# Kernel tuning notes

Measured on AMD Instinct MI355X. Metric: run time of the kernel, lower is better.

## Reference

```python
import jax, jax.numpy as jnp
import numpy as np
import math

MAX_DEGREE = 20
K = (MAX_DEGREE + 1) ** 2  # 441
RANK = 256
N = 262144


def _spharm_all(inc, azim):
    """Real spherical harmonics Y_lm(inc, azim) for all l<=MAX_DEGREE, -l<=m<=l.
    Matches the standard real SH used by get_spherical_harmonics_element:
      Y_l0  = N_l0 * P_l^0(cos inc)
      Y_lm  = sqrt(2) * N_lm * P_l^m(cos inc) * cos(m*azim),  m>0
      Y_l-m = sqrt(2) * N_lm * P_l^m(cos inc) * sin(m*azim),  m>0
    with Condon-Shortley phase folded into the associated Legendre recurrence.
    Output layout: index l*(l+1)+m (the flax index map of the module).
    Returns [..., K]."""
    x = jnp.cos(inc)
    s = jnp.sin(inc)
    # Associated Legendre P_l^m(x) via standard recurrences (trace-time loops,
    # fused by XLA into one elementwise program).
    P = {(0, 0): jnp.ones_like(x)}
    for m in range(1, MAX_DEGREE + 1):
        P[(m, m)] = -(2 * m - 1) * s * P[(m - 1, m - 1)]  # Condon-Shortley
    for m in range(0, MAX_DEGREE):
        P[(m + 1, m)] = (2 * m + 1) * x * P[(m, m)]
    for m in range(0, MAX_DEGREE + 1):
        for l in range(m + 2, MAX_DEGREE + 1):
            P[(l, m)] = ((2 * l - 1) * x * P[(l - 1, m)] - (l + m - 1) * P[(l - 2, m)]) / (l - m)

    cols = [None] * K
    for l in range(MAX_DEGREE + 1):
        for m in range(-l, l + 1):
            am = abs(m)
            norm = math.sqrt((2 * l + 1) / (4.0 * math.pi)
                             * math.factorial(l - am) / math.factorial(l + am))
            if m == 0:
                y = norm * P[(l, 0)]
            elif m > 0:
                y = (math.sqrt(2.0) * norm) * P[(l, am)] * jnp.cos(am * azim)
            else:
                y = (math.sqrt(2.0) * norm) * P[(l, am)] * jnp.sin(am * azim)
            cols[l * (l + 1) + m] = y
    return jnp.stack(cols, axis=-1)


def _cart2sphere(O):
    # returns (azimuth, inclination) of 3-vectors O[..., 3]
    r = jnp.linalg.norm(O, axis=-1)
    azim = jnp.arctan2(O[..., 1], O[..., 0])
    inc = jnp.arccos(jnp.clip(O[..., 2] / r, -1.0, 1.0))
    return azim, inc


def setup_inputs() -> dict:
    key = jax.random.key(0)
    k1, k2, k3 = jax.random.split(key, 3)
    coordinates = jax.random.normal(k1, (N, 6), dtype=jnp.float32)
    rand_i = jax.random.randint(k2, (RANK,), 0, K, dtype=jnp.int32)
    rand_j = jax.random.randint(k3, (RANK,), 0, K, dtype=jnp.int32)
    return {"coordinates": coordinates, "rand_i": rand_i, "rand_j": rand_j}


def reference(coordinates, rand_i, rand_j):
    a1, i1 = _cart2sphere(coordinates[..., :3])
    a2, i2 = _cart2sphere(coordinates[..., 3:])
    Psi_1 = _spharm_all(i1, a1)  # [..., K]
    Psi_2 = _spharm_all(i2, a2)  # [..., K]
    # rank random (i,j) pairs: gathered elementwise product -> [..., RANK]
    return jnp.take(Psi_1, rand_i, axis=-1) * jnp.take(Psi_2, rand_j, axis=-1)
```

## Files before the change

### kernel.cpp

```cpp
#include <hip/hip_runtime.h>
#include <math.h>

#define MAXDEG 20
#define NM 21
#define RANK 256
#define PPB 12
#define NSLOT (2*PPB)
#define S_STRIDE 446
#define HDRS 65


__device__ __forceinline__ int remap_idx(int k) {
  int l = (int)sqrtf((float)k);
  if (l*l > k) --l;
  if ((l+1)*(l+1) <= k) ++l;
  int m = k - l*(l+1);
  int am = m < 0 ? -m : m;
  if (am == 0) return 420 + l;
  return (am-1)*(42-am) + 2*(l-am) + (m < 0 ? 1 : 0);
}

__global__ __launch_bounds__(256, 3)
void sh_fused(const float* __restrict__ coords,
              const int* __restrict__ rand_i,
              const int* __restrict__ rand_j,
              float* __restrict__ out, int N) {
  __shared__ float2 s_ab[231];
  __shared__ float  s_hdr[NSLOT * HDRS];
  __shared__ float  s_tab[NSLOT * S_STRIDE];

  const int t  = threadIdx.x;
  const int n0 = blockIdx.x * PPB;

  const int ri = remap_idx(rand_i[t]);
  const int rj = remap_idx(rand_j[t]);

  if (t < 231) {
    int l = (int)((sqrtf(8.0f*(float)t + 1.0f) - 1.0f) * 0.5f);
    if (l*(l+1)/2 > t) --l;
    if ((l+1)*(l+2)/2 <= t) ++l;
    int m = t - l*(l+1)/2;
    float a = 0.f, b = 0.f;
    if (l >= m + 2) {
      float l2 = (float)(l*l), m2 = (float)(m*m);
      float inv = 1.0f / (l2 - m2);
      a = sqrtf((4.f*l2 - 1.f) * inv);
      b = sqrtf((2.f*(float)l + 1.f) * ((float)((l-1)*(l-1)) - m2)
                / (2.f*(float)l - 3.f) * inv);
    }
    s_ab[t] = make_float2(a, b);
  }

  if (t < NSLOT) {
    int p = t >> 1, d = t & 1;
    int n = n0 + p; if (n >= N) n = N - 1;
    const float* c = coords + (size_t)n * 6 + d * 3;
    float cx = c[0], cy = c[1], cz = c[2];
    float r2 = cx*cx + cy*cy + cz*cz;
    float x = cz * rsqrtf(r2);
    x = fminf(1.f, fmaxf(-1.f, x));
    float s = sqrtf(fmaxf(0.f, 1.f - x*x));
    float rho2 = cx*cx + cy*cy;
    float cphi, sphi;
    if (rho2 > 0.f) { float ir = rsqrtf(rho2); cphi = cx*ir; sphi = cy*ir; }
    else            { cphi = 1.f; sphi = 0.f; }
    float* h = s_hdr + t * HDRS;
    float cm = 1.f, sm = 0.f;
    float pmm = 0.28209479177387814f;
    h[0] = 1.f; h[21] = 0.f; h[42] = pmm; h[63] = x;
    for (int m = 1; m <= MAXDEG; ++m) {
      float cn = cm*cphi - sm*sphi;
      float sn = sm*cphi + cm*sphi;
      cm = cn; sm = sn;
      float df = -sqrtf((2.f*(float)m + 1.f) / (2.f*(float)m));
      if (m == 1) df *= 1.41421356237309515f;
      pmm = df * s * pmm;
      h[m] = cm; h[21+m] = sm; h[42+m] = pmm;
    }
  }
  __syncthreads();

  for (int task = t; task < NM * NSLOT; task += 256) {
    int m  = task / NSLOT;
    int pd = task - m * NSLOT;
    const float* h = s_hdr + pd * HDRS;
    float x  = h[63];
    float cm = h[m], sm = h[21+m], p1 = h[42+m];
    float* slot = s_tab + pd * S_STRIDE;
    if (m == 0) {
      float* col = slot + 420;
      col[0] = p1;
      float p2 = p1;
      float p = 1.7320508075688772f * x * p1;
      col[1] = p;
      int ti = 3;
      for (int l = 2; l <= MAXDEG; ++l) {
        float2 ab = s_ab[ti];
        float pn = ab.x * (x * p) - ab.y * p2;
        p2 = p; p = pn;
        col[l] = pn;
        ti += l + 1;
      }
    } else {
      float2* col = (float2*)(slot + (m-1)*(42-m));
      col[0] = make_float2(p1*cm, p1*sm);
      if (m < MAXDEG) {
        float p2 = p1;
        float p = sqrtf(2.f*(float)m + 3.f) * x * p1;
        col[1] = make_float2(p*cm, p*sm);
        int ti = (m+2)*(m+3)/2 + m;
        for (int l = m+2; l <= MAXDEG; ++l) {
          float2 ab = s_ab[ti];
          float pn = ab.x * (x * p) - ab.y * p2;
          p2 = p; p = pn;
          col[l-m] = make_float2(pn*cm, pn*sm);
          ti += l + 1;
        }
      }
    }
  }
  __syncthreads();

  for (int p = 0; p < PPB; ++p) {
    int n = n0 + p;
    if (n < N) {
      float v = s_tab[(2*p)*S_STRIDE + ri] * s_tab[(2*p+1)*S_STRIDE + rj];
      out[(size_t)n * RANK + t] = v;
    }
  }
}

extern "C" void kernel_launch(void* const* d_in, const int* in_sizes, int n_in,
                              void* d_out, int out_size, void* d_ws, size_t ws_size,
                              hipStream_t stream) {
  const float* coords = (const float*)d_in[0];
  const int*   rand_i = (const int*)d_in[1];
  const int*   rand_j = (const int*)d_in[2];
  float*       out    = (float*)d_out;
  const int N = in_sizes[0] / 6;
  const int grid = (N + PPB - 1) / PPB;
  sh_fused<<<grid, 256, 0, stream>>>(coords, rand_i, rand_j, out, N);
}
```

Before: 394.0 us.

## Parallelize header setup per m, pair Legendre chains, vectorize output stores

Reduces points per block from 12 to 8 and raises the launch-bounds occupancy hint. The serial per-slot header recurrence (cos/sin and P_mm) is replaced by closed forms (atan2 plus sincos of m*phi, and exp2 of m*log2(s)), so all threads compute headers in parallel instead of 16 threads looping over m. Each thread now runs two Legendre chains, one for each direction of a point, and the output is written as float4 using four remapped indices per thread. This cuts the serial prologue and widens the global stores, at the cost of fast-math approximations (__sincosf, exp2/log2) that may lose accuracy at higher m.

After: 437.4 us. +11.0%, slower.

```diff
diff --git a/kernel.cpp b/kernel.cpp
--- a/kernel.cpp
+++ b/kernel.cpp
@@ -4,7 +4,7 @@
 #define MAXDEG 20
 #define NM 21
 #define RANK 256
-#define PPB 12
+#define PPB 8
 #define NSLOT (2*PPB)
 #define S_STRIDE 446
 #define HDRS 65
@@ -20,7 +20,7 @@
   return (am-1)*(42-am) + 2*(l-am) + (m < 0 ? 1 : 0);
 }
 
-__global__ __launch_bounds__(256, 3)
+__global__ __launch_bounds__(256, 4)
 void sh_fused(const float* __restrict__ coords,
               const int* __restrict__ rand_i,
               const int* __restrict__ rand_j,
@@ -32,8 +32,14 @@
   const int t  = threadIdx.x;
   const int n0 = blockIdx.x * PPB;
 
-  const int ri = remap_idx(rand_i[t]);
-  const int rj = remap_idx(rand_j[t]);
+  const int rg = t & 63;
+  int rI[4], rJ[4];
+  {
+    int4 a = ((const int4*)rand_i)[rg];
+    int4 b = ((const int4*)rand_j)[rg];
+    rI[0]=remap_idx(a.x); rI[1]=remap_idx(a.y); rI[2]=remap_idx(a.z); rI[3]=remap_idx(a.w);
+    rJ[0]=remap_idx(b.x); rJ[1]=remap_idx(b.y); rJ[2]=remap_idx(b.z); rJ[3]=remap_idx(b.w);
+  }
 
   if (t < 231) {
     int l = (int)((sqrtf(8.0f*(float)t + 1.0f) - 1.0f) * 0.5f);
@@ -51,82 +57,98 @@
     s_ab[t] = make_float2(a, b);
   }
 
-  if (t < NSLOT) {
-    int p = t >> 1, d = t & 1;
+  {
+    const int slot = t & 15;
+    const int p = slot >> 1, d = slot & 1;
     int n = n0 + p; if (n >= N) n = N - 1;
     const float* c = coords + (size_t)n * 6 + d * 3;
     float cx = c[0], cy = c[1], cz = c[2];
-    float r2 = cx*cx + cy*cy + cz*cz;
-    float x = cz * rsqrtf(r2);
+    float x = cz * rsqrtf(cx*cx + cy*cy + cz*cz);
     x = fminf(1.f, fmaxf(-1.f, x));
     float s = sqrtf(fmaxf(0.f, 1.f - x*x));
-    float rho2 = cx*cx + cy*cy;
-    float cphi, sphi;
-    if (rho2 > 0.f) { float ir = rsqrtf(rho2); cphi = cx*ir; sphi = cy*ir; }
-    else            { cphi = 1.f; sphi = 0.f; }
-    float* h = s_hdr + t * HDRS;
-    float cm = 1.f, sm = 0.f;
-    float pmm = 0.28209479177387814f;
-    h[0] = 1.f; h[21] = 0.f; h[42] = pmm; h[63] = x;
-    for (int m = 1; m <= MAXDEG; ++m) {
-      float cn = cm*cphi - sm*sphi;
-      float sn = sm*cphi + cm*sphi;
-      cm = cn; sm = sn;
-      float df = -sqrtf((2.f*(float)m + 1.f) / (2.f*(float)m));
-      if (m == 1) df *= 1.41421356237309515f;
-      pmm = df * s * pmm;
-      h[m] = cm; h[21+m] = sm; h[42+m] = pmm;
+    s = fmaxf(s, 1e-30f);
+    float phi = atan2f(cy, cx);
+    float l2s = log2f(s);
+    float* h = s_hdr + slot * HDRS;
+    if ((t >> 4) == 0) h[63] = x;
+    for (int m = (t >> 4); m < NM; m += 16) {
+      float sv, cv;
+      __sincosf((float)m * phi, &sv, &cv);
+      float prod = 1.f;
+      for (int k = 1; k <= m; ++k) prod *= (2.f*(float)k + 1.f) / (2.f*(float)k);
+      float Km = 0.28209479177387814f * sqrtf(prod);
+      if (m > 0) { Km *= 1.41421356237309515f; if (m & 1) Km = -Km; }
+      float pmm = Km * exp2f((float)m * l2s);
+      h[m] = cv; h[21 + m] = sv; h[42 + m] = pmm;
     }
   }
   __syncthreads();
 
-  for (int task = t; task < NM * NSLOT; task += 256) {
-    int m  = task / NSLOT;
-    int pd = task - m * NSLOT;
-    const float* h = s_hdr + pd * HDRS;
-    float x  = h[63];
-    float cm = h[m], sm = h[21+m], p1 = h[42+m];
-    float* slot = s_tab + pd * S_STRIDE;
+  if (t < NM * PPB) {
+    const int m = t >> 3, p = t & 7;
+    const float* h0 = s_hdr + (2*p) * HDRS;
+    const float* h1 = h0 + HDRS;
+    float x0 = h0[63],   x1 = h1[63];
+    float cm0 = h0[m],   sm0 = h0[21+m], pm0 = h0[42+m];
+    float cm1 = h1[m],   sm1 = h1[21+m], pm1 = h1[42+m];
+    float* slot0 = s_tab + (2*p) * S_STRIDE;
+    float* slot1 = slot0 + S_STRIDE;
     if (m == 0) {
-      float* col = slot + 420;
-      col[0] = p1;
-      float p2 = p1;
-      float p = 1.7320508075688772f * x * p1;
-      col[1] = p;
+      float* c0 = slot0 + 420; float* c1 = slot1 + 420;
+      float q0 = pm0, q1 = pm1;
+      c0[0] = q0; c1[0] = q1;
+      float p0 = 1.7320508075688772f * x0 * q0;
+      float p1 = 1.7320508075688772f * x1 * q1;
+      c0[1] = p0; c1[1] = p1;
       int ti = 3;
       for (int l = 2; l <= MAXDEG; ++l) {
         float2 ab = s_ab[ti];
-        float pn = ab.x * (x * p) - ab.y * p2;
-        p2 = p; p = pn;
-        col[l] = pn;
+        float v0 = ab.x * (x0 * p0) - ab.y * q0;
+        float v1 = ab.x * (x1 * p1) - ab.y * q1;
+        q0 = p0; p0 = v0; q1 = p1; p1 = v1;
+        c0[l] = v0; c1[l] = v1;
         ti += l + 1;
       }
     } else {
-      float2* col = (float2*)(slot + (m-1)*(42-m));
-      col[0] = make_float2(p1*cm, p1*sm);
+      const int cb = (m-1)*(42-m);
+      float2* c0 = (float2*)(slot0 + cb);
+      float2* c1 = (float2*)(slot1 + cb);
+      c0[0] = make_float2(pm0*cm0, pm0*sm0);
+      c1[0] = make_float2(pm1*cm1, pm1*sm1);
       if (m < MAXDEG) {
-        float p2 = p1;
-        float p = sqrtf(2.f*(float)m + 3.f) * x * p1;
-        col[1] = make_float2(p*cm, p*sm);
+        float q0 = pm0, q1 = pm1;
+        float se = sqrtf(2.f*(float)m + 3.f);
+        float p0 = se * x0 * pm0, p1 = se * x1 * pm1;
+        c0[1] = make_float2(p0*cm0, p0*sm0);
+        c1[1] = make_float2(p1*cm1, p1*sm1);
         int ti = (m+2)*(m+3)/2 + m;
+        int idx = 2;
         for (int l = m+2; l <= MAXDEG; ++l) {
           float2 ab = s_ab[ti];
-          float pn = ab.x * (x * p) - ab.y * p2;
-          p2 = p; p = pn;
-          col[l-m] = make_float2(pn*cm, pn*sm);
-          ti += l + 1;
+          float v0 = ab.x * (x0 * p0) - ab.y * q0;
+          float v1 = ab.x * (x1 * p1) - ab.y * q1;
+          q0 = p0; p0 = v0; q1 = p1; p1 = v1;
+          c0[idx] = make_float2(v0*cm0, v0*sm0);
+          c1[idx] = make_float2(v1*cm1, v1*sm1);
+          ++idx; ti += l + 1;
         }
       }
     }
   }
   __syncthreads();
 
-  for (int p = 0; p < PPB; ++p) {
-    int n = n0 + p;
-    if (n < N) {
-      float v = s_tab[(2*p)*S_STRIDE + ri] * s_tab[(2*p+1)*S_STRIDE + rj];
-      out[(size_t)n * RANK + t] = v;
-    }
+  const int pi = t >> 6;
+  for (int k = 0; k < PPB/4; ++k) {
+    const int p = pi + 4*k;
+    const float* Y1 = s_tab + (2*p) * S_STRIDE;
+    const float* Y2 = Y1 + S_STRIDE;
+    float4 v;
+    v.x = Y1[rI[0]] * Y2[rJ[0]];
+    v.y = Y1[rI[1]] * Y2[rJ[1]];
+    v.z = Y1[rI[2]] * Y2[rJ[2]];
+    v.w = Y1[rI[3]] * Y2[rJ[3]];
+    const int n = n0 + p;
+    if (n < N) *(float4*)(out + (size_t)n * RANK + 4*rg) = v;
   }
 }
 
```
